# Optimization experiments

Measured on AMD Instinct MI355X. Metric: run time of the kernel, lower is better.

Reference implementation:

```python
import jax, jax.numpy as jnp
import numpy as np

D_MODEL = 2048
D_INNER = 2048
N_QK = 32
N_V = 32
D_STATE = 64
D_CONV = 4
CHUNK = 128
CONV_DIM = D_INNER + 2 * N_QK * D_STATE  # 6144
IN_OUT = 2 * D_INNER + 2 * N_QK * D_STATE + N_V  # 8224


def setup_inputs() -> dict:
    key = jax.random.key(0)
    ks = jax.random.split(key, 6)
    u = jax.random.normal(ks[0], (2, 4096, D_MODEL), dtype=jnp.float32)
    W_in = jax.random.normal(ks[1], (IN_OUT, D_MODEL), dtype=jnp.float32) * 0.02
    conv_w = jax.random.normal(ks[2], (CONV_DIM, D_CONV), dtype=jnp.float32) * 0.2
    conv_b = jax.random.normal(ks[3], (CONV_DIM,), dtype=jnp.float32) * 0.02
    D = jnp.ones((N_V,), dtype=jnp.float32)
    z_bias = jnp.zeros((D_INNER,), dtype=jnp.float32)
    W_out = jax.random.normal(ks[4], (D_MODEL, D_INNER), dtype=jnp.float32) * 0.02
    return {"u": u, "W_in": W_in, "conv_w": conv_w, "conv_b": conv_b,
            "D": D, "z_bias": z_bias, "W_out": W_out}


def causal_depthwise_conv(x, w, b):
    # x: [B, L, C]; w: [C, K]; b: [C]. Torch Conv1d(groups=C, padding=K-1)[..., :L]
    B, L, C = x.shape
    K = w.shape[1]
    xp = jnp.pad(x, ((0, 0), (K - 1, 0), (0, 0)))
    y = b[None, None, :]
    for k in range(K):
        y = y + xp[:, k:k + L, :] * w[None, None, :, k]
    return y


def ssd_chunk_scan(x, dt, B, C, chunk):
    # Mamba2 SSD with A = -1 per head.
    # x: [b,l,h,p], dt: [b,l,h] (positive), B,C: [b,l,h,n]
    b, l, h, p = x.shape
    n = B.shape[-1]
    nc = l // chunk
    x = x.reshape(b, nc, chunk, h, p)
    dt = dt.reshape(b, nc, chunk, h)
    B = B.reshape(b, nc, chunk, h, n)
    C = C.reshape(b, nc, chunk, h, n)
    a = -dt                                  # A * dt
    cum = jnp.cumsum(a, axis=2)              # [b,nc,q,h]
    xdt = x * dt[..., None]                  # dt_t * x_t
    # ---- intra-chunk (causal, decay exp(cum_q - cum_k), q >= k) ----
    CB = jnp.einsum('bcqhn,bckhn->bchqk', C, B)
    cumT = jnp.swapaxes(cum, 2, 3)           # [b,nc,h,q]
    diff = cumT[..., :, None] - cumT[..., None, :]   # [b,nc,h,q,k]
    mask = jnp.tril(jnp.ones((chunk, chunk), dtype=bool))
    decay = jnp.exp(jnp.where(mask, diff, -jnp.inf))
    y_intra = jnp.einsum('bchqk,bckhp->bcqhp', CB * decay, xdt)
    # ---- per-chunk final states ----
    state_decay = jnp.exp(cum[:, :, -1:, :] - cum)   # [b,nc,q,h]
    states = jnp.einsum('bckhn,bckhp->bchpn', B * state_decay[..., None], xdt)
    chunk_decay = jnp.exp(cum[:, :, -1, :])          # [b,nc,h]
    # ---- inter-chunk recurrence ----
    def step(carry, inp):
        st, cd = inp  # st [b,h,p,n], cd [b,h]
        new = carry * cd[:, :, None, None] + st
        return new, carry  # emit the state *entering* this chunk
    init = jnp.zeros((b, h, p, n), dtype=x.dtype)
    _, prev = jax.lax.scan(step, init,
                           (jnp.moveaxis(states, 1, 0), jnp.moveaxis(chunk_decay, 1, 0)))
    prev = jnp.moveaxis(prev, 0, 1)                  # [b,nc,h,p,n]
    y_inter = jnp.einsum('bcqhn,bchpn->bcqhp', C * jnp.exp(cum)[..., None], prev)
    return (y_intra + y_inter).reshape(b, l, h, p)


def reference(u, W_in, conv_w, conv_b, D, z_bias, W_out):
    b, l, _ = u.shape  # l divisible by CHUNK (padded_len == l)
    xBCzA = jnp.einsum('bld,od->blo', u, W_in)
    xBC = xBCzA[..., :CONV_DIM]
    z = xBCzA[..., CONV_DIM:CONV_DIM + D_INNER]
    A_log = xBCzA[..., CONV_DIM + D_INNER:]
    xBC = causal_depthwise_conv(xBC, conv_w, conv_b)  # activation = identity
    x = xBC[..., :D_INNER]
    Bm = xBC[..., D_INNER:D_INNER + N_QK * D_STATE]
    Cm = xBC[..., D_INNER + N_QK * D_STATE:]
    x = x.reshape(b, l, N_V, D_INNER // N_V)
    Bm = Bm.reshape(b, l, N_QK, D_STATE)
    Cm = Cm.reshape(b, l, N_QK, D_STATE)
    dt = jax.nn.softplus(A_log)                       # [b,l,h]
    x_scan = x / dt[..., None]
    y = ssd_chunk_scan(x_scan, dt, Bm, Cm, CHUNK)
    y = y + D[None, None, :, None] * x                # Du uses undivided x
    y = y.reshape(b, l, D_INNER)
    out = jnp.einsum('bli,oi->blo', y * jax.nn.silu(z + z_bias), W_out)
    return out
```

## Files before the change

kernel.cpp:

```cpp
#include <hip/hip_runtime.h>
#include <math.h>

#define D_MODEL  2048
#define D_INNER  2048
#define N_QK     32
#define N_V      32
#define D_STATE  64
#define D_CONV   4
#define CHUNK    128
#define CONV_DIM 6144
#define IN_OUT   8224
#define BATCH    2
#define SEQ      4096
#define M_ROWS   (BATCH*SEQ)
#define NCHUNK   (SEQ/CHUNK)

typedef unsigned short bf16_t;
typedef __attribute__((ext_vector_type(4))) float f32x4;
typedef __attribute__((ext_vector_type(8))) short bf16x8;

#define SWZ64(r,c)  ((((r)*64)  + (c)) ^ (((r)&7)<<3))
#define SWZ128(r,c) ((((r)*128) + (c)) ^ (((r)&7)<<3))

__device__ __forceinline__ float b2f(bf16_t u) {
    union { unsigned int i; float f; } w; w.i = ((unsigned int)u) << 16; return w.f;
}
__device__ __forceinline__ bf16_t f2b(float f) {
    unsigned int x = __float_as_uint(f);
    return (bf16_t)((x + 0x7FFFu + ((x >> 16) & 1u)) >> 16);
}
__device__ __forceinline__ void store4b(bf16_t* dst, float4 v) {
    ushort4 u; u.x = f2b(v.x); u.y = f2b(v.y); u.z = f2b(v.z); u.w = f2b(v.w);
    *reinterpret_cast<ushort4*>(dst) = u;
}

__device__ __forceinline__ void gload_lds16(const bf16_t* g, bf16_t* l) {
    __builtin_amdgcn_global_load_lds((const __attribute__((address_space(1))) void*)g,
                                     (__attribute__((address_space(3))) void*)l,
                                     16, 0, 0);
}

__global__ __launch_bounds__(256) void f2b_kernel(const float* __restrict__ in,
                                                  bf16_t* __restrict__ out, long n)
{
    const long i = ((long)blockIdx.x * 256 + threadIdx.x) * 4;
    if (i < n) {
        float4 v = *reinterpret_cast<const float4*>(in + i);
        ushort4 o;
        o.x = f2b(v.x); o.y = f2b(v.y); o.z = f2b(v.z); o.w = f2b(v.w);
        *reinterpret_cast<ushort4*>(out + i) = o;
    }
}

template<int NTB, int K, bool OBF16>
__global__ __launch_bounds__(512, 2) void gemm256(const bf16_t* __restrict__ A,
                                                  const bf16_t* __restrict__ B,
                                                  void* __restrict__ Cv,
                                                  long ldc)
{
    constexpr int BK = 64;
    constexpr int NT = K / BK;
    __shared__ bf16_t As[2][256 * BK];
    __shared__ bf16_t Bs[2][256 * BK];

    const int nwg = gridDim.x;
    const int bid = blockIdx.x;
    const int wg  = ((nwg & 7) == 0) ? ((bid & 7) * (nwg >> 3) + (bid >> 3)) : bid;
    const int bm = (wg / NTB) * 256;
    const int bn = (wg % NTB) * 256;

    const int tid  = threadIdx.x;
    const int lane = tid & 63;
    const int wv   = tid >> 6;
    const int wr   = wv >> 2, wc = wv & 3;
    const int l15  = lane & 15, l4 = lane >> 4;

    f32x4 acc[8][4];
    #pragma unroll
    for (int i = 0; i < 8; ++i)
        #pragma unroll
        for (int j = 0; j < 4; ++j) acc[i][j] = (f32x4){0.f, 0.f, 0.f, 0.f};

    const bf16_t* Abase = A + (long)bm * K;
    const bf16_t* Bbase = B + (long)bn * K;

    auto stage = [&](int t, int buf) {
        const bf16_t* Ab = Abase + t * BK;
        const bf16_t* Bb = Bbase + t * BK;
        #pragma unroll
        for (int it = 0; it < 4; ++it) {
            const int seg = it * 512 + tid;
            const int row = seg >> 3, c16 = seg & 7;
            const int sc = (c16 ^ (row & 7)) * 8;
            gload_lds16(Ab + (long)row * K + sc, &As[buf][seg * 8]);
            gload_lds16(Bb + (long)row * K + sc, &Bs[buf][seg * 8]);
        }
    };

    stage(0, 0);
    asm volatile("s_waitcnt vmcnt(0)" ::: "memory");
    __builtin_amdgcn_s_barrier();

    for (int t = 0; t < NT; ++t) {
        const int cur = t & 1;
        if (t + 1 < NT) stage(t + 1, cur ^ 1);
        bf16x8 bfr[4], af[4];
        #pragma unroll
        for (int ks = 0; ks < 2; ++ks) {
            #pragma unroll
            for (int ni = 0; ni < 4; ++ni) {
                const int row = wc * 64 + ni * 16 + l15;
                const int ch = (ks * 4 + l4) ^ (row & 7);
                bfr[ni] = *reinterpret_cast<const bf16x8*>(&Bs[cur][row * 64 + ch * 8]);
            }
            #pragma unroll
            for (int qm = 0; qm < 2; ++qm) {
                #pragma unroll
                for (int mi = 0; mi < 4; ++mi) {
                    const int row = wr * 128 + qm * 64 + mi * 16 + l15;
                    const int ch = (ks * 4 + l4) ^ (row & 7);
                    af[mi] = *reinterpret_cast<const bf16x8*>(&As[cur][row * 64 + ch * 8]);
                }
                __builtin_amdgcn_s_setprio(1);
                #pragma unroll
                for (int mi = 0; mi < 4; ++mi)
                    #pragma unroll
                    for (int ni = 0; ni < 4; ++ni)
                        acc[qm * 4 + mi][ni] = __builtin_amdgcn_mfma_f32_16x16x32_bf16(
                            af[mi], bfr[ni], acc[qm * 4 + mi][ni], 0, 0, 0);
                __builtin_amdgcn_s_setprio(0);
                if (ks * 2 + qm < 3) __builtin_amdgcn_s_barrier();
            }
        }
        asm volatile("s_waitcnt vmcnt(0)" ::: "memory");
        __builtin_amdgcn_s_barrier();
    }

    #pragma unroll
    for (int mf = 0; mf < 8; ++mf) {
        const long grow0 = bm + wr * 128 + mf * 16 + l4 * 4;
        #pragma unroll
        for (int ni = 0; ni < 4; ++ni) {
            const int gcol = bn + wc * 64 + ni * 16 + l15;
            #pragma unroll
            for (int j = 0; j < 4; ++j) {
                if (OBF16)
                    ((bf16_t*)Cv)[(grow0 + j) * ldc + gcol] = f2b(acc[mf][ni][j]);
                else
                    ((float*)Cv)[(grow0 + j) * ldc + gcol] = acc[mf][ni][j];
            }
        }
    }
}

template<int N, int K, bool OBF16>
__global__ __launch_bounds__(256) void gemm_mfma(const bf16_t* __restrict__ A,
                                                 const bf16_t* __restrict__ B,
                                                 void* __restrict__ Cv,
                                                 long ldc)
{
    constexpr int BM = 128, BN = 128, BK = 64;
    constexpr int NTB = (N + BN - 1) / BN;
    __shared__ bf16_t As[BM * BK];
    __shared__ bf16_t Bs[BM * BK];

    const int nwg = gridDim.x;
    const int bid = blockIdx.x;
    const int wg  = ((nwg & 7) == 0) ? ((bid & 7) * (nwg >> 3) + (bid >> 3)) : bid;
    const int bm = (wg / NTB) * BM;
    const int bn = (wg % NTB) * BN;

    const int tid  = threadIdx.x;
    const int lane = tid & 63;
    const int wv   = tid >> 6;
    const int wr   = wv >> 1, wc = wv & 1;

    f32x4 acc[4][4];
    #pragma unroll
    for (int i = 0; i < 4; ++i)
        #pragma unroll
        for (int j = 0; j < 4; ++j) acc[i][j] = (f32x4){0.f, 0.f, 0.f, 0.f};

    for (int k0 = 0; k0 < K; k0 += BK) {
        #pragma unroll
        for (int it = 0; it < 4; ++it) {
            const int seg = it * 256 + tid;
            const int row = seg >> 3, c16 = seg & 7;
            gload_lds16(A + (long)(bm + row) * K + k0 + c16 * 8,
                        &As[row * BK + c16 * 8]);
            int brow = bn + row;
            if constexpr (N % BN != 0) brow = min(brow, N - 1);
            gload_lds16(B + (long)brow * K + k0 + c16 * 8,
                        &Bs[row * BK + c16 * 8]);
        }
        __syncthreads();
        #pragma unroll
        for (int kk = 0; kk < 2; ++kk) {
            bf16x8 af[4], bfr[4];
            const int kc = kk * 32 + (lane >> 4) * 8;
            #pragma unroll
            for (int mi = 0; mi < 4; ++mi) {
                const int row = wr * 64 + mi * 16 + (lane & 15);
                af[mi] = *reinterpret_cast<const bf16x8*>(&As[row * BK + kc]);
            }
            #pragma unroll
            for (int ni = 0; ni < 4; ++ni) {
                const int row = wc * 64 + ni * 16 + (lane & 15);
                bfr[ni] = *reinterpret_cast<const bf16x8*>(&Bs[row * BK + kc]);
            }
            #pragma unroll
            for (int mi = 0; mi < 4; ++mi)
                #pragma unroll
                for (int ni = 0; ni < 4; ++ni)
                    acc[mi][ni] = __builtin_amdgcn_mfma_f32_16x16x32_bf16(
                        af[mi], bfr[ni], acc[mi][ni], 0, 0, 0);
        }
        __syncthreads();
    }

    #pragma unroll
    for (int mi = 0; mi < 4; ++mi) {
        const long row0 = bm + wr * 64 + mi * 16 + ((lane >> 4) << 2);
        #pragma unroll
        for (int ni = 0; ni < 4; ++ni) {
            const int col = bn + wc * 64 + ni * 16 + (lane & 15);
            if (N % BN != 0 && col >= N) continue;
            #pragma unroll
            for (int j = 0; j < 4; ++j) {
                if (OBF16)
                    ((bf16_t*)Cv)[(row0 + j) * ldc + col] = f2b(acc[mi][ni][j]);
                else
                    ((float*)Cv)[(row0 + j) * ldc + col] = acc[mi][ni][j];
            }
        }
    }
}

__device__ __forceinline__ float4 conv4v(const bf16_t* __restrict__ xb, long m, int l,
                                         int col, const float* __restrict__ cw,
                                         const float* __restrict__ cbv)
{
    float4 acc = *reinterpret_cast<const float4*>(cbv + col);
    float4 wc0 = *reinterpret_cast<const float4*>(cw + (long)col * 4);
    float4 wc1 = *reinterpret_cast<const float4*>(cw + (long)col * 4 + 4);
    float4 wc2 = *reinterpret_cast<const float4*>(cw + (long)col * 4 + 8);
    float4 wc3 = *reinterpret_cast<const float4*>(cw + (long)col * 4 + 12);
    const float t0[4] = {wc0.x, wc0.y, wc0.z, wc0.w};
    const float t1[4] = {wc1.x, wc1.y, wc1.z, wc1.w};
    const float t2[4] = {wc2.x, wc2.y, wc2.z, wc2.w};
    const float t3[4] = {wc3.x, wc3.y, wc3.z, wc3.w};
    #pragma unroll
    for (int tap = 0; tap < 4; ++tap) {
        if (l - 3 + tap < 0) continue;
        const bf16_t* p = xb + (m - 3 + tap) * (long)IN_OUT + col;
        ushort4 v = *reinterpret_cast<const ushort4*>(p);
        acc.x = fmaf(b2f(v.x), t0[tap], acc.x);
        acc.y = fmaf(b2f(v.y), t1[tap], acc.y);
        acc.z = fmaf(b2f(v.z), t2[tap], acc.z);
        acc.w = fmaf(b2f(v.w), t3[tap], acc.w);
    }
    return acc;
}

__global__ __launch_bounds__(256) void dt_kernel(const bf16_t* __restrict__ xb,
                                                 float* __restrict__ dt)
{
    const int i = blockIdx.x * 256 + threadIdx.x;
    if (i < M_ROWS * N_V) {
        const int m = i >> 5, h = i & 31;
        const float a = b2f(xb[(long)m * IN_OUT + (CONV_DIM + D_INNER) + h]);
        dt[i] = (a > 20.f) ? a : log1pf(expf(a));
    }
}

__global__ __launch_bounds__(256) void ssd_states(const bf16_t* __restrict__ xb,
                                                  const float* __restrict__ dt,
                                                  const float* __restrict__ cw,
                                                  const float* __restrict__ cbv,
                                                  float* __restrict__ states,
                                                  float* __restrict__ cumbuf,
                                                  float* __restrict__ cdecay)
{
    const int h = blockIdx.x, c = blockIdx.y, b = blockIdx.z;
    __shared__ float sB[CHUNK][68];
    __shared__ float sx[CHUNK][68];
    __shared__ float cum[CHUNK];
    const int t = threadIdx.x;
    const long mbase = (long)b * SEQ + (long)c * CHUNK;
    if (t < CHUNK) cum[t] = -dt[(mbase + t) * N_V + h];
    for (int idx = t; idx < CHUNK * 16; idx += 256) {
        const int k = idx >> 4, q4 = (idx & 15) * 4;
        const long m = mbase + k;
        const int l = (int)(m & (SEQ - 1));
        float4 xv = conv4v(xb, m, l, h * 64 + q4, cw, cbv);
        float4 bv = conv4v(xb, m, l, D_INNER + h * 64 + q4, cw, cbv);
        *reinterpret_cast<float4*>(&sx[k][q4]) = xv;
        *reinterpret_cast<float4*>(&sB[k][q4]) = bv;
    }
    __syncthreads();
    if (t == 0) { float s = 0.f; for (int k = 0; k < CHUNK; ++k) { s += cum[k]; cum[k] = s; } }
    __syncthreads();
    const float clast = cum[CHUNK - 1];
    const int p = t >> 2, n0 = (t & 3) * 16;
    float acc[16];
    #pragma unroll
    for (int j = 0; j < 16; ++j) acc[j] = 0.f;
    for (int k = 0; k < CHUNK; ++k) {
        const float sxk = sx[k][p] * __expf(clast - cum[k]);
        #pragma unroll
        for (int j = 0; j < 16; ++j) acc[j] = fmaf(sB[k][n0 + j], sxk, acc[j]);
    }
    const long cb = ((long)b * NCHUNK + c) * N_QK + h;
    const long sbase = (cb * 64 + p) * 64 + n0;
    #pragma unroll
    for (int j = 0; j < 16; ++j) states[sbase + j] = acc[j];
    if (t < CHUNK) cumbuf[cb * CHUNK + t] = cum[t];
    if (t == 0)   cdecay[cb] = __expf(clast);
}

__global__ __launch_bounds__(256) void ssd_scan(float* __restrict__ states,
                                                const float* __restrict__ cdecay)
{
    const int bh = blockIdx.x;
    const int b = bh >> 5, h = bh & 31;
    const int t = threadIdx.x;
    float carry[16];
    #pragma unroll
    for (int j = 0; j < 16; ++j) carry[j] = 0.f;
    for (int c = 0; c < NCHUNK; ++c) {
        const long cb = ((long)b * NCHUNK + c) * N_QK + h;
        const long base = cb * 4096 + (long)t * 16;
        const float cd = cdecay[cb];
        #pragma unroll
        for (int v = 0; v < 4; ++v) {
            float4 st = *reinterpret_cast<const float4*>(&states[base + v * 4]);
            float4 pv = make_float4(carry[v*4], carry[v*4+1], carry[v*4+2], carry[v*4+3]);
            *reinterpret_cast<float4*>(&states[base + v * 4]) = pv;
            carry[v*4]   = fmaf(carry[v*4],   cd, st.x);
            carry[v*4+1] = fmaf(carry[v*4+1], cd, st.y);
            carry[v*4+2] = fmaf(carry[v*4+2], cd, st.z);
            carry[v*4+3] = fmaf(carry[v*4+3], cd, st.w);
        }
    }
}

__global__ __launch_bounds__(256) void ssd_out(const bf16_t* __restrict__ xb,
                                               const float* __restrict__ cumbuf,
                                               const float* __restrict__ prevst,
                                               const float* __restrict__ Dvec,
                                               const float* __restrict__ zbias,
                                               const float* __restrict__ cw,
                                               const float* __restrict__ cbv,
                                               bf16_t* __restrict__ yz)
{
    const int h = blockIdx.x, c = blockIdx.y, b = blockIdx.z;
    __shared__ bf16_t sC[128 * 64];
    __shared__ bf16_t sB[128 * 64];
    __shared__ bf16_t sXQ[128 * 64];
    __shared__ bf16_t sXT[64 * 128];
    __shared__ bf16_t sP[64 * 64];
    __shared__ float  cum[CHUNK];
    const int t = threadIdx.x;
    const long mbase = (long)b * SEQ + (long)c * CHUNK;
    const long cb = ((long)b * NCHUNK + c) * N_QK + h;
    if (t < CHUNK) cum[t] = cumbuf[cb * CHUNK + t];
    for (int idx = t; idx < CHUNK * 16; idx += 256) {
        const int k = idx >> 4, q4 = (idx & 15) * 4;
        const long m = mbase + k;
        const int l = (int)(m & (SEQ - 1));
        float4 xv = conv4v(xb, m, l, h * 64 + q4, cw, cbv);
        float4 bv = conv4v(xb, m, l, D_INNER + h * 64 + q4, cw, cbv);
        float4 cv = conv4v(xb, m, l, 2 * D_INNER + h * 64 + q4, cw, cbv);
        store4b(&sXQ[SWZ64(k, q4)], xv);
        store4b(&sB [SWZ64(k, q4)], bv);
        store4b(&sC [SWZ64(k, q4)], cv);
    }
    for (int idx = t; idx < 64 * 16; idx += 256) {
        const int p = idx >> 4, q4 = (idx & 15) * 4;
        float4 v = *reinterpret_cast<const float4*>(prevst + cb * 4096 + p * 64 + q4);
        store4b(&sP[SWZ64(p, q4)], v);
    }
    __syncthreads();
    {
        const int j = t & 127;
        const int c8b = (t >> 7) * 4;
        #pragma unroll
        for (int it = 0; it < 4; ++it) {
            const int c8 = c8b + it;
            bf16x8 v = *reinterpret_cast<const bf16x8*>(&sXQ[SWZ64(j, c8 * 8)]);
            #pragma unroll
            for (int e = 0; e < 8; ++e) sXT[SWZ128(c8 * 8 + e, j)] = v[e];
        }
    }
    __syncthreads();

    const int lane = t & 63, wv = t >> 6;
    const int w32 = wv * 32, l15 = lane & 15, l4 = lane >> 4;
    bf16_t* sQ = sXQ;

    f32x4 yac[2][4], iac[2][4];
    #pragma unroll
    for (int mi = 0; mi < 2; ++mi)
        #pragma unroll
        for (int np = 0; np < 4; ++np) {
            yac[mi][np] = (f32x4){0.f, 0.f, 0.f, 0.f};
            iac[mi][np] = (f32x4){0.f, 0.f, 0.f, 0.f};
        }

    #pragma unroll
    for (int H = 0; H < 2; ++H) {
        if (H == 1 && wv < 2) break;
        const int j0 = H * 64;
        f32x4 sac[2][4];
        #pragma unroll
        for (int mi = 0; mi < 2; ++mi)
            #pragma unroll
            for (int nj = 0; nj < 4; ++nj) sac[mi][nj] = (f32x4){0.f, 0.f, 0.f, 0.f};
        #pragma unroll
        for (int kk = 0; kk < 2; ++kk) {
            const int kc = kk * 32 + l4 * 8;
            bf16x8 af0 = *reinterpret_cast<const bf16x8*>(&sC[SWZ64(w32 + l15, kc)]);
            bf16x8 af1 = *reinterpret_cast<const bf16x8*>(&sC[SWZ64(w32 + 16 + l15, kc)]);
            #pragma unroll
            for (int nj = 0; nj < 4; ++nj) {
                bf16x8 bfj = *reinterpret_cast<const bf16x8*>(&sB[SWZ64(j0 + nj * 16 + l15, kc)]);
                if (j0 + nj * 16 <= w32 + 15)
                    sac[0][nj] = __builtin_amdgcn_mfma_f32_16x16x32_bf16(af0, bfj, sac[0][nj], 0, 0, 0);
                if (j0 + nj * 16 <= w32 + 31)
                    sac[1][nj] = __builtin_amdgcn_mfma_f32_16x16x32_bf16(af1, bfj, sac[1][nj], 0, 0, 0);
            }
        }
        #pragma unroll
        for (int mi = 0; mi < 2; ++mi) {
            #pragma unroll
            for (int nj = 0; nj < 4; ++nj) {
                const int jcol = nj * 16 + l15;
                const int jg = j0 + jcol;
                #pragma unroll
                for (int jj = 0; jj < 4; ++jj) {
                    const int i = w32 + mi * 16 + l4 * 4 + jj;
                    const float q = (jg <= i) ? __expf(cum[i] - cum[jg]) * sac[mi][nj][jj] : 0.f;
                    sQ[SWZ64(i, jcol)] = f2b(q);
                }
            }
        }
        #pragma unroll
        for (int kk = 0; kk < 2; ++kk) {
            const int kc = kk * 32 + l4 * 8;
            bf16x8 qa0 = *reinterpret_cast<const bf16x8*>(&sQ[SWZ64(w32 + l15, kc)]);
            bf16x8 qa1 = *reinterpret_cast<const bf16x8*>(&sQ[SWZ64(w32 + 16 + l15, kc)]);
            #pragma unroll
            for (int np = 0; np < 4; ++np) {
                bf16x8 xf = *reinterpret_cast<const bf16x8*>(&sXT[SWZ128(np * 16 + l15, j0 + kc)]);
                yac[0][np] = __builtin_amdgcn_mfma_f32_16x16x32_bf16(qa0, xf, yac[0][np], 0, 0, 0);
                yac[1][np] = __builtin_amdgcn_mfma_f32_16x16x32_bf16(qa1, xf, yac[1][np], 0, 0, 0);
            }
        }
    }
    #pragma unroll
    for (int kk = 0; kk < 2; ++kk) {
        const int kc = kk * 32 + l4 * 8;
        bf16x8 cf0 = *reinterpret_cast<const bf16x8*>(&sC[SWZ64(w32 + l15, kc)]);
        bf16x8 cf1 = *reinterpret_cast<const bf16x8*>(&sC[SWZ64(w32 + 16 + l15, kc)]);
        #pragma unroll
        for (int np = 0; np < 4; ++np) {
            bf16x8 pf = *reinterpret_cast<const bf16x8*>(&sP[SWZ64(np * 16 + l15, kc)]);
            iac[0][np] = __builtin_amdgcn_mfma_f32_16x16x32_bf16(cf0, pf, iac[0][np], 0, 0, 0);
            iac[1][np] = __builtin_amdgcn_mfma_f32_16x16x32_bf16(cf1, pf, iac[1][np], 0, 0, 0);
        }
    }
    const float dh = Dvec[h];
    #pragma unroll
    for (int mi = 0; mi < 2; ++mi) {
        #pragma unroll
        for (int jj = 0; jj < 4; ++jj) {
            const int i = w32 + mi * 16 + l4 * 4 + jj;
            const float ei = __expf(cum[i]);
            const long m = mbase + i;
            const bf16_t* zr = xb + m * (long)IN_OUT + CONV_DIM + h * 64;
            bf16_t* orow = yz + m * (long)D_INNER + h * 64;
            #pragma unroll
            for (int np = 0; np < 4; ++np) {
                const int p = np * 16 + l15;
                const float xval = b2f(sXT[SWZ128(p, i)]);
                const float y = yac[mi][np][jj] + ei * iac[mi][np][jj] + dh * xval;
                const float zv = b2f(zr[p]) + zbias[h * 64 + p];
                const float s = zv / (1.f + __expf(-zv));
                orow[p] = f2b(y * s);
            }
        }
    }
}

extern "C" void kernel_launch(void* const* d_in, const int* in_sizes, int n_in,
                              void* d_out, int out_size, void* d_ws, size_t ws_size,
                              hipStream_t stream)
{
    const float* u      = (const float*)d_in[0];
    const float* W_in   = (const float*)d_in[1];
    const float* conv_w = (const float*)d_in[2];
    const float* conv_b = (const float*)d_in[3];
    const float* Dv     = (const float*)d_in[4];
    const float* z_bias = (const float*)d_in[5];
    const float* W_out  = (const float*)d_in[6];
    float* out = (float*)d_out;

    char* w = (char*)d_ws;
    bf16_t* xbcza = (bf16_t*)w;  w += (long)M_ROWS * IN_OUT * 2;
    bf16_t* wob   = (bf16_t*)w;  w += (long)2048 * 2048 * 2;
    char* ureg = w;
    bf16_t* ub  = (bf16_t*)ureg;
    bf16_t* wib = (bf16_t*)(ureg + (long)M_ROWS * D_MODEL * 2);
    bf16_t* yzb = (bf16_t*)ureg;
    float*  dtb = (float*)(ureg + (long)M_ROWS * D_INNER * 2);
    float*  cumb   = dtb + (long)M_ROWS * N_V;
    float*  states = cumb + (long)BATCH * NCHUNK * N_QK * CHUNK;
    float*  cdec   = states + (long)BATCH * NCHUNK * N_QK * 4096;

    f2b_kernel<<<(int)(((long)M_ROWS * D_MODEL / 4 + 255) / 256), 256, 0, stream>>>(
        u, ub, (long)M_ROWS * D_MODEL);
    f2b_kernel<<<(int)(((long)IN_OUT * D_MODEL / 4 + 255) / 256), 256, 0, stream>>>(
        W_in, wib, (long)IN_OUT * D_MODEL);
    f2b_kernel<<<(int)(((long)D_MODEL * D_INNER / 4 + 255) / 256), 256, 0, stream>>>(
        W_out, wob, (long)D_MODEL * D_INNER);

    gemm256<32, D_MODEL, true><<<(M_ROWS / 256) * 32, 512, 0, stream>>>(
        ub, wib, xbcza, IN_OUT);
    gemm_mfma<32, D_MODEL, true><<<(M_ROWS / 128), 256, 0, stream>>>(
        ub, wib + (long)8192 * D_MODEL, xbcza + 8192, IN_OUT);

    dt_kernel<<<(M_ROWS * N_V + 255) / 256, 256, 0, stream>>>(xbcza, dtb);

    ssd_states<<<dim3(N_QK, NCHUNK, BATCH), 256, 0, stream>>>(xbcza, dtb, conv_w, conv_b,
                                                              states, cumb, cdec);

    ssd_scan<<<BATCH * N_QK, 256, 0, stream>>>(states, cdec);

    ssd_out<<<dim3(N_QK, NCHUNK, BATCH), 256, 0, stream>>>(xbcza, cumb, states, Dv, z_bias,
                                                           conv_w, conv_b, yzb);

    gemm256<8, D_INNER, false><<<(M_ROWS / 256) * 8, 512, 0, stream>>>(
        yzb, wob, out, D_MODEL);
}
```

Measured before the change: 867.6 us.

## Merge tail GEMM, fuse dt into ssd_states, use MFMA for chunk states, widen scan

The separate 128x128 tail GEMM over the last 32 columns is dropped, and the 256-tile GEMM gets a tail-clamped 33rd column tile that covers all 8224 outputs in one launch. The dt_kernel is fused into ssd_states, which now computes softplus inline, uses a parallel prefix scan for the cumulative sum, and replaces scalar FMA state accumulation with bf16 MFMA over transposed LDS tiles. The inter-chunk scan is split across four times as many blocks. The tail tile wastes most of its MFMA work on clamped rows, and bf16 rounding of the decayed B values lowers precision.

Measured after the change: 837.9 us. 1.04x faster.

```diff
diff --git a/kernel.cpp b/kernel.cpp
--- a/kernel.cpp
+++ b/kernel.cpp
@@ -52,14 +52,15 @@
     }
 }
 
-template<int NTB, int K, bool OBF16>
+template<int NTB, int K, bool OBF16, int NCOLS>
 __global__ __launch_bounds__(512, 2) void gemm256(const bf16_t* __restrict__ A,
                                                   const bf16_t* __restrict__ B,
-                                                  void* __restrict__ Cv,
-                                                  long ldc)
+                                                  void* __restrict__ Cv)
 {
     constexpr int BK = 64;
     constexpr int NT = K / BK;
+    constexpr bool HASTAIL = (NTB * 256 > NCOLS);
+    const long ldc = NCOLS;
     __shared__ bf16_t As[2][256 * BK];
     __shared__ bf16_t Bs[2][256 * BK];
 
@@ -82,18 +83,18 @@
         for (int j = 0; j < 4; ++j) acc[i][j] = (f32x4){0.f, 0.f, 0.f, 0.f};
 
     const bf16_t* Abase = A + (long)bm * K;
-    const bf16_t* Bbase = B + (long)bn * K;
 
     auto stage = [&](int t, int buf) {
         const bf16_t* Ab = Abase + t * BK;
-        const bf16_t* Bb = Bbase + t * BK;
         #pragma unroll
         for (int it = 0; it < 4; ++it) {
             const int seg = it * 512 + tid;
             const int row = seg >> 3, c16 = seg & 7;
             const int sc = (c16 ^ (row & 7)) * 8;
             gload_lds16(Ab + (long)row * K + sc, &As[buf][seg * 8]);
-            gload_lds16(Bb + (long)row * K + sc, &Bs[buf][seg * 8]);
+            int br = bn + row;
+            if (HASTAIL) br = min(br, NCOLS - 1);
+            gload_lds16(B + (long)br * K + t * BK + sc, &Bs[buf][seg * 8]);
         }
     };
 
@@ -142,95 +143,13 @@
         #pragma unroll
         for (int ni = 0; ni < 4; ++ni) {
             const int gcol = bn + wc * 64 + ni * 16 + l15;
+            if (HASTAIL && gcol >= NCOLS) continue;
             #pragma unroll
             for (int j = 0; j < 4; ++j) {
                 if (OBF16)
                     ((bf16_t*)Cv)[(grow0 + j) * ldc + gcol] = f2b(acc[mf][ni][j]);
                 else
                     ((float*)Cv)[(grow0 + j) * ldc + gcol] = acc[mf][ni][j];
-            }
-        }
-    }
-}
-
-template<int N, int K, bool OBF16>
-__global__ __launch_bounds__(256) void gemm_mfma(const bf16_t* __restrict__ A,
-                                                 const bf16_t* __restrict__ B,
-                                                 void* __restrict__ Cv,
-                                                 long ldc)
-{
-    constexpr int BM = 128, BN = 128, BK = 64;
-    constexpr int NTB = (N + BN - 1) / BN;
-    __shared__ bf16_t As[BM * BK];
-    __shared__ bf16_t Bs[BM * BK];
-
-    const int nwg = gridDim.x;
-    const int bid = blockIdx.x;
-    const int wg  = ((nwg & 7) == 0) ? ((bid & 7) * (nwg >> 3) + (bid >> 3)) : bid;
-    const int bm = (wg / NTB) * BM;
-    const int bn = (wg % NTB) * BN;
-
-    const int tid  = threadIdx.x;
-    const int lane = tid & 63;
-    const int wv   = tid >> 6;
-    const int wr   = wv >> 1, wc = wv & 1;
-
-    f32x4 acc[4][4];
-    #pragma unroll
-    for (int i = 0; i < 4; ++i)
-        #pragma unroll
-        for (int j = 0; j < 4; ++j) acc[i][j] = (f32x4){0.f, 0.f, 0.f, 0.f};
-
-    for (int k0 = 0; k0 < K; k0 += BK) {
-        #pragma unroll
-        for (int it = 0; it < 4; ++it) {
-            const int seg = it * 256 + tid;
-            const int row = seg >> 3, c16 = seg & 7;
-            gload_lds16(A + (long)(bm + row) * K + k0 + c16 * 8,
-                        &As[row * BK + c16 * 8]);
-            int brow = bn + row;
-            if constexpr (N % BN != 0) brow = min(brow, N - 1);
-            gload_lds16(B + (long)brow * K + k0 + c16 * 8,
-                        &Bs[row * BK + c16 * 8]);
-        }
-        __syncthreads();
-        #pragma unroll
-        for (int kk = 0; kk < 2; ++kk) {
-            bf16x8 af[4], bfr[4];
-            const int kc = kk * 32 + (lane >> 4) * 8;
-            #pragma unroll
-            for (int mi = 0; mi < 4; ++mi) {
-                const int row = wr * 64 + mi * 16 + (lane & 15);
-                af[mi] = *reinterpret_cast<const bf16x8*>(&As[row * BK + kc]);
-            }
-            #pragma unroll
-            for (int ni = 0; ni < 4; ++ni) {
-                const int row = wc * 64 + ni * 16 + (lane & 15);
-                bfr[ni] = *reinterpret_cast<const bf16x8*>(&Bs[row * BK + kc]);
-            }
-            #pragma unroll
-            for (int mi = 0; mi < 4; ++mi)
-                #pragma unroll
-                for (int ni = 0; ni < 4; ++ni)
-                    acc[mi][ni] = __builtin_amdgcn_mfma_f32_16x16x32_bf16(
-                        af[mi], bfr[ni], acc[mi][ni], 0, 0, 0);
-        }
-        __syncthreads();
-    }
-
-    #pragma unroll
-    for (int mi = 0; mi < 4; ++mi) {
-        const long row0 = bm + wr * 64 + mi * 16 + ((lane >> 4) << 2);
-        #pragma unroll
-        for (int ni = 0; ni < 4; ++ni) {
-            const int col = bn + wc * 64 + ni * 16 + (lane & 15);
-            if (N % BN != 0 && col >= N) continue;
-            #pragma unroll
-            for (int j = 0; j < 4; ++j) {
-                if (OBF16)
-                    ((bf16_t*)Cv)[(row0 + j) * ldc + col] = f2b(acc[mi][ni][j]);
-                else
-                    ((float*)Cv)[(row0 + j) * ldc + col] = acc[mi][ni][j];
             }
         }
     }
@@ -262,19 +181,7 @@
     return acc;
 }
 
-__global__ __launch_bounds__(256) void dt_kernel(const bf16_t* __restrict__ xb,
-                                                 float* __restrict__ dt)
-{
-    const int i = blockIdx.x * 256 + threadIdx.x;
-    if (i < M_ROWS * N_V) {
-        const int m = i >> 5, h = i & 31;
-        const float a = b2f(xb[(long)m * IN_OUT + (CONV_DIM + D_INNER) + h]);
-        dt[i] = (a > 20.f) ? a : log1pf(expf(a));
-    }
-}
-
 __global__ __launch_bounds__(256) void ssd_states(const bf16_t* __restrict__ xb,
-                                                  const float* __restrict__ dt,
                                                   const float* __restrict__ cw,
                                                   const float* __restrict__ cbv,
                                                   float* __restrict__ states,
@@ -282,38 +189,79 @@
                                                   float* __restrict__ cdecay)
 {
     const int h = blockIdx.x, c = blockIdx.y, b = blockIdx.z;
-    __shared__ float sB[CHUNK][68];
-    __shared__ float sx[CHUNK][68];
-    __shared__ float cum[CHUNK];
+    __shared__ bf16_t sx [128 * 64];
+    __shared__ bf16_t sBr[128 * 64];
+    __shared__ bf16_t sXT[64 * 128];
+    __shared__ bf16_t sBT[64 * 128];
+    __shared__ float  cum[CHUNK];
     const int t = threadIdx.x;
     const long mbase = (long)b * SEQ + (long)c * CHUNK;
-    if (t < CHUNK) cum[t] = -dt[(mbase + t) * N_V + h];
+    const long cb = ((long)b * NCHUNK + c) * N_QK + h;
+
+    if (t < CHUNK) {
+        const float a = b2f(xb[(mbase + t) * (long)IN_OUT + (CONV_DIM + D_INNER) + h]);
+        cum[t] = -((a > 20.f) ? a : log1pf(expf(a)));
+    }
     for (int idx = t; idx < CHUNK * 16; idx += 256) {
         const int k = idx >> 4, q4 = (idx & 15) * 4;
         const long m = mbase + k;
         const int l = (int)(m & (SEQ - 1));
         float4 xv = conv4v(xb, m, l, h * 64 + q4, cw, cbv);
         float4 bv = conv4v(xb, m, l, D_INNER + h * 64 + q4, cw, cbv);
-        *reinterpret_cast<float4*>(&sx[k][q4]) = xv;
-        *reinterpret_cast<float4*>(&sB[k][q4]) = bv;
+        store4b(&sx [SWZ64(k, q4)], xv);
+        store4b(&sBr[SWZ64(k, q4)], bv);
     }
     __syncthreads();
-    if (t == 0) { float s = 0.f; for (int k = 0; k < CHUNK; ++k) { s += cum[k]; cum[k] = s; } }
+    #pragma unroll
+    for (int s = 1; s < CHUNK; s <<= 1) {
+        float pv = 0.f;
+        if (t < CHUNK && t >= s) pv = cum[t - s];
+        __syncthreads();
+        if (t < CHUNK && t >= s) cum[t] += pv;
+        __syncthreads();
+    }
+    const float clast = cum[CHUNK - 1];
+    {
+        const int j = t & 127;
+        const int c8b = (t >> 7) * 4;
+        const float ej = __expf(clast - cum[j]);
+        #pragma unroll
+        for (int it = 0; it < 4; ++it) {
+            const int c8 = c8b + it;
+            bf16x8 xv = *reinterpret_cast<const bf16x8*>(&sx [SWZ64(j, c8 * 8)]);
+            bf16x8 bv = *reinterpret_cast<const bf16x8*>(&sBr[SWZ64(j, c8 * 8)]);
+            #pragma unroll
+            for (int e = 0; e < 8; ++e) {
+                sXT[SWZ128(c8 * 8 + e, j)] = xv[e];
+                sBT[SWZ128(c8 * 8 + e, j)] = f2b(b2f((bf16_t)bv[e]) * ej);
+            }
+        }
+    }
     __syncthreads();
-    const float clast = cum[CHUNK - 1];
-    const int p = t >> 2, n0 = (t & 3) * 16;
-    float acc[16];
-    #pragma unroll
-    for (int j = 0; j < 16; ++j) acc[j] = 0.f;
-    for (int k = 0; k < CHUNK; ++k) {
-        const float sxk = sx[k][p] * __expf(clast - cum[k]);
-        #pragma unroll
-        for (int j = 0; j < 16; ++j) acc[j] = fmaf(sB[k][n0 + j], sxk, acc[j]);
-    }
-    const long cb = ((long)b * NCHUNK + c) * N_QK + h;
-    const long sbase = (cb * 64 + p) * 64 + n0;
-    #pragma unroll
-    for (int j = 0; j < 16; ++j) states[sbase + j] = acc[j];
+
+    const int lane = t & 63, wv = t >> 6;
+    const int l15 = lane & 15, l4 = lane >> 4;
+    f32x4 acc[4];
+    #pragma unroll
+    for (int nj = 0; nj < 4; ++nj) acc[nj] = (f32x4){0.f, 0.f, 0.f, 0.f};
+    #pragma unroll
+    for (int ks = 0; ks < 4; ++ks) {
+        const int kc = ks * 32 + l4 * 8;
+        bf16x8 af = *reinterpret_cast<const bf16x8*>(&sXT[SWZ128(wv * 16 + l15, kc)]);
+        #pragma unroll
+        for (int nj = 0; nj < 4; ++nj) {
+            bf16x8 bf = *reinterpret_cast<const bf16x8*>(&sBT[SWZ128(nj * 16 + l15, kc)]);
+            acc[nj] = __builtin_amdgcn_mfma_f32_16x16x32_bf16(af, bf, acc[nj], 0, 0, 0);
+        }
+    }
+    #pragma unroll
+    for (int nj = 0; nj < 4; ++nj) {
+        #pragma unroll
+        for (int jj = 0; jj < 4; ++jj) {
+            const int p = wv * 16 + l4 * 4 + jj;
+            states[cb * 4096 + (long)p * 64 + nj * 16 + l15] = acc[nj][jj];
+        }
+    }
     if (t < CHUNK) cumbuf[cb * CHUNK + t] = cum[t];
     if (t == 0)   cdecay[cb] = __expf(clast);
 }
@@ -321,26 +269,22 @@
 __global__ __launch_bounds__(256) void ssd_scan(float* __restrict__ states,
                                                 const float* __restrict__ cdecay)
 {
-    const int bh = blockIdx.x;
+    const int bid = blockIdx.x;
+    const int bh = bid >> 2, q = bid & 3;
     const int b = bh >> 5, h = bh & 31;
     const int t = threadIdx.x;
-    float carry[16];
-    #pragma unroll
-    for (int j = 0; j < 16; ++j) carry[j] = 0.f;
+    const int off = q * 1024 + t * 4;
+    float4 carry = make_float4(0.f, 0.f, 0.f, 0.f);
     for (int c = 0; c < NCHUNK; ++c) {
         const long cb = ((long)b * NCHUNK + c) * N_QK + h;
-        const long base = cb * 4096 + (long)t * 16;
+        const long base = cb * 4096 + off;
         const float cd = cdecay[cb];
-        #pragma unroll
-        for (int v = 0; v < 4; ++v) {
-            float4 st = *reinterpret_cast<const float4*>(&states[base + v * 4]);
-            float4 pv = make_float4(carry[v*4], carry[v*4+1], carry[v*4+2], carry[v*4+3]);
-            *reinterpret_cast<float4*>(&states[base + v * 4]) = pv;
-            carry[v*4]   = fmaf(carry[v*4],   cd, st.x);
-            carry[v*4+1] = fmaf(carry[v*4+1], cd, st.y);
-            carry[v*4+2] = fmaf(carry[v*4+2], cd, st.z);
-            carry[v*4+3] = fmaf(carry[v*4+3], cd, st.w);
-        }
+        float4 st = *reinterpret_cast<const float4*>(&states[base]);
+        *reinterpret_cast<float4*>(&states[base]) = carry;
+        carry.x = fmaf(carry.x, cd, st.x);
+        carry.y = fmaf(carry.y, cd, st.y);
+        carry.z = fmaf(carry.z, cd, st.z);
+        carry.w = fmaf(carry.w, cd, st.w);
     }
 }
 
@@ -512,8 +456,7 @@
     bf16_t* ub  = (bf16_t*)ureg;
     bf16_t* wib = (bf16_t*)(ureg + (long)M_ROWS * D_MODEL * 2);
     bf16_t* yzb = (bf16_t*)ureg;
-    float*  dtb = (float*)(ureg + (long)M_ROWS * D_INNER * 2);
-    float*  cumb   = dtb + (long)M_ROWS * N_V;
+    float*  cumb   = (float*)(ureg + (long)M_ROWS * D_INNER * 2);
     float*  states = cumb + (long)BATCH * NCHUNK * N_QK * CHUNK;
     float*  cdec   = states + (long)BATCH * NCHUNK * N_QK * 4096;
 
@@ -524,21 +467,17 @@
     f2b_kernel<<<(int)(((long)D_MODEL * D_INNER / 4 + 255) / 256), 256, 0, stream>>>(
         W_out, wob, (long)D_MODEL * D_INNER);
 
-    gemm256<32, D_MODEL, true><<<(M_ROWS / 256) * 32, 512, 0, stream>>>(
-        ub, wib, xbcza, IN_OUT);
-    gemm_mfma<32, D_MODEL, true><<<(M_ROWS / 128), 256, 0, stream>>>(
-        ub, wib + (long)8192 * D_MODEL, xbcza + 8192, IN_OUT);
-
-    dt_kernel<<<(M_ROWS * N_V + 255) / 256, 256, 0, stream>>>(xbcza, dtb);
-
-    ssd_states<<<dim3(N_QK, NCHUNK, BATCH), 256, 0, stream>>>(xbcza, dtb, conv_w, conv_b,
+    gemm256<33, D_MODEL, true, IN_OUT><<<(M_ROWS / 256) * 33, 512, 0, stream>>>(
+        ub, wib, xbcza);
+
+    ssd_states<<<dim3(N_QK, NCHUNK, BATCH), 256, 0, stream>>>(xbcza, conv_w, conv_b,
                                                               states, cumb, cdec);
 
-    ssd_scan<<<BATCH * N_QK, 256, 0, stream>>>(states, cdec);
+    ssd_scan<<<BATCH * N_QK * 4, 256, 0, stream>>>(states, cdec);
 
     ssd_out<<<dim3(N_QK, NCHUNK, BATCH), 256, 0, stream>>>(xbcza, cumb, states, Dv, z_bias,
                                                            conv_w, conv_b, yzb);
 
-    gemm256<8, D_INNER, false><<<(M_ROWS / 256) * 8, 512, 0, stream>>>(
-        yzb, wob, out, D_MODEL);
-}
+    gemm256<8, D_INNER, false, D_MODEL><<<(M_ROWS / 256) * 8, 512, 0, stream>>>(
+        yzb, wob, out);
+}
```
